# Performance work log

Measured on AMD Instinct MI355X. Metric: run time of the kernel, lower is better.

The kernel has to match this reference:

```python
import jax, jax.numpy as jnp
import numpy as np
from jax import lax

BATCH = 8192
HID = 10
IN = 64
STEPS = 512
REVERSE = True


def setup_inputs() -> dict:
    key = jax.random.key(0)
    ks = jax.random.split(key, 9)
    s_in = 1.0 / np.sqrt(HID)
    return {
        "hidden": jax.random.normal(ks[0], (1, BATCH, HID), dtype=jnp.float32),
        "w_ih": jax.random.uniform(ks[1], (3 * HID, IN), jnp.float32, -s_in, s_in),
        "w_hh": jax.random.uniform(ks[2], (3 * HID, HID), jnp.float32, -s_in, s_in),
        "b_ih": jax.random.uniform(ks[3], (3 * HID,), jnp.float32, -s_in, s_in),
        "b_hh": jax.random.uniform(ks[4], (3 * HID,), jnp.float32, -s_in, s_in),
        "l1_w": jax.random.uniform(ks[5], (10, HID), jnp.float32, -s_in, s_in),
        "l1_b": jax.random.uniform(ks[6], (10,), jnp.float32, -s_in, s_in),
        "l2_w": jax.random.uniform(ks[7], (IN, 10), jnp.float32, -s_in, s_in),
        "l2_b": jax.random.uniform(ks[8], (IN,), jnp.float32, -s_in, s_in),
        "step": STEPS,
    }


def _gru_cell(h, x, w_ih, w_hh, b_ih, b_hh):
    # PyTorch GRU gate order: reset, update, new
    gi = x @ w_ih.T + b_ih  # [B, 3H]
    gh = h @ w_hh.T + b_hh  # [B, 3H]
    i_r, i_z, i_n = jnp.split(gi, 3, axis=-1)
    h_r, h_z, h_n = jnp.split(gh, 3, axis=-1)
    r = jax.nn.sigmoid(i_r + h_r)
    z = jax.nn.sigmoid(i_z + h_z)
    n = jnp.tanh(i_n + r * h_n)
    return (1.0 - z) * n + z * h


def reference(hidden, w_ih, w_hh, b_ih, b_hh, l1_w, l1_b, l2_w, l2_b, step):
    h0 = hidden[0]  # [B, H]
    B = h0.shape[0]
    x0 = jnp.zeros((B, IN), dtype=h0.dtype)  # first GRU input is zeros

    def body(carry, _):
        h, x = carry
        h_new = _gru_cell(h, x, w_ih, w_hh, b_ih, b_hh)
        o = h_new @ l1_w.T + l1_b          # l1 on GRU output
        x_next = o @ l2_w.T + l2_b         # l2 feeds next GRU step
        return (h_new, x_next), o

    _, outs = lax.scan(body, (h0, x0), None, length=step)  # [T, B, 10]
    outs = jnp.transpose(outs, (1, 0, 2))  # [B, T, 10]
    if REVERSE:
        outs = outs[:, ::-1, :]
    return outs
```

## Files before the change

### kernel.cpp

```cpp
#include <hip/hip_runtime.h>

#define HID 10
#define STEPS 512

typedef __attribute__((ext_vector_type(2))) float v2f;

template<int F>
static __device__ __forceinline__ float swz(float v) {
    return __int_as_float(__builtin_amdgcn_ds_swizzle(__float_as_int(v), (F << 5) | 0x10));
}

__global__ __launch_bounds__(64, 2) void gru_decoder_kernel(
    const float* __restrict__ hidden, const float* __restrict__ w_ih,
    const float* __restrict__ w_hh, const float* __restrict__ b_ih,
    const float* __restrict__ b_hh, const float* __restrict__ l1_w,
    const float* __restrict__ l1_b, const float* __restrict__ l2_w,
    const float* __restrict__ l2_b, float* __restrict__ out)
{
    __shared__ float sWx[640];
    __shared__ float sbx[64];
    __shared__ float sWgi[300];
    __shared__ float sbgi[30];
    __shared__ float sWhh[300];

    const int lane = threadIdx.x;
    const int f    = lane & 15;
    const int b    = blockIdx.x * 4 + (lane >> 4);
    const bool ok  = (f < HID);
    const int fi   = ok ? f : 0;

    for (int e = lane; e < 640; e += 64) {
        int i = e / 10, j = e - i * 10;
        float acc = 0.f;
        #pragma unroll
        for (int k = 0; k < 10; ++k) acc += l2_w[i * 10 + k] * l1_w[k * 10 + j];
        sWx[e] = acc;
    }
    {
        float acc = l2_b[lane];
        #pragma unroll
        for (int k = 0; k < 10; ++k) acc += l2_w[lane * 10 + k] * l1_b[k];
        sbx[lane] = acc;
    }
    for (int e = lane; e < 300; e += 64) sWhh[e] = w_hh[e];
    __syncthreads();
    for (int e = lane; e < 300; e += 64) {
        int m = e / 10, j = e - m * 10;
        float acc = 0.f;
        for (int k = 0; k < 64; ++k) acc += w_ih[m * 64 + k] * sWx[k * 10 + j];
        sWgi[e] = acc;
    }
    if (lane < 30) {
        float acc = b_ih[lane];
        for (int k = 0; k < 64; ++k) acc += w_ih[lane * 64 + k] * sbx[k];
        sbgi[lane] = acc;
    }
    __syncthreads();

    const float LOG2E = 1.4426950408889634f;
    const float S2    = 2.f * LOG2E;

    v2f wrz[10], wnn[10];
    float wo[10];
    #pragma unroll
    for (int k = 0; k < 10; ++k) {
        float grz_r = -(sWgi[fi * 10 + k] + sWhh[fi * 10 + k]) * LOG2E;
        float grz_z = -(sWgi[(10 + fi) * 10 + k] + sWhh[(10 + fi) * 10 + k]) * LOG2E;
        float gni   = sWgi[(20 + fi) * 10 + k] * S2;
        float gnh   = sWhh[(20 + fi) * 10 + k] * S2;
        wrz[k] = ok ? v2f{grz_r, grz_z} : v2f{0.f, 0.f};
        wnn[k] = ok ? v2f{gni, gnh} : v2f{0.f, 0.f};
        wo[k]  = ok ? l1_w[fi * 10 + k] : 0.f;
    }
    const v2f brz = ok ? v2f{-(sbgi[fi] + b_hh[fi]) * LOG2E,
                             -(sbgi[10 + fi] + b_hh[10 + fi]) * LOG2E}
                       : v2f{0.f, 0.f};
    const v2f bnn = ok ? v2f{sbgi[20 + fi] * S2, b_hh[20 + fi] * S2} : v2f{0.f, 0.f};
    const float bo = ok ? l1_b[fi] : 0.f;
    const v2f brz0 = ok ? v2f{-(b_ih[fi] + b_hh[fi]) * LOG2E,
                              -(b_ih[10 + fi] + b_hh[10 + fi]) * LOG2E}
                        : v2f{0.f, 0.f};
    const float bni0 = ok ? b_ih[20 + fi] * S2 : 0.f;

    float h = ok ? hidden[(size_t)b * HID + f] : 0.f;

    float ha[10];
    #define GATHER()                                                       \
        ha[0] = swz<0>(h); ha[1] = swz<1>(h); ha[2] = swz<2>(h);           \
        ha[3] = swz<3>(h); ha[4] = swz<4>(h); ha[5] = swz<5>(h);           \
        ha[6] = swz<6>(h); ha[7] = swz<7>(h); ha[8] = swz<8>(h);           \
        ha[9] = swz<9>(h);

    GATHER();

    float* pb = out + (size_t)b * (STEPS * HID) + (size_t)(STEPS - 1) * HID + f;

    #define O_AND_STORE()                                                  \
        {                                                                  \
            float o = bo;                                                  \
            _Pragma("unroll")                                              \
            for (int k = 0; k < 10; ++k) o += wo[k] * ha[k];               \
            if (ok) pb[0] = o;                                             \
            pb -= HID;                                                     \
        }

    {
        float pr = 0.f, pz = 0.f, ph = 0.f;
        #pragma unroll
        for (int k = 0; k < 10; ++k) {
            pr += sWhh[fi * 10 + k] * ha[k];
            pz += sWhh[(10 + fi) * 10 + k] * ha[k];
            ph += sWhh[(20 + fi) * 10 + k] * ha[k];
        }
        float vr = brz0.x - pr * LOG2E;
        float vz = brz0.y - pz * LOG2E;
        float r = __builtin_amdgcn_rcpf(1.f + __builtin_amdgcn_exp2f(vr));
        float z = __builtin_amdgcn_rcpf(1.f + __builtin_amdgcn_exp2f(vz));
        float y = bni0 + r * (ph * S2 + bnn.y);
        float n = 1.f - 2.f * __builtin_amdgcn_rcpf(1.f + __builtin_amdgcn_exp2f(y));
        h = ok ? (n + z * (h - n)) : 0.f;
        GATHER();
        O_AND_STORE();
    }

    #pragma unroll 1
    for (int t = 1; t < STEPS; ++t) {
        v2f arz = brz, ann = bnn;
        #pragma unroll
        for (int k = 0; k < 10; ++k) {
            v2f hh = {ha[k], ha[k]};
            arz += wrz[k] * hh;
            ann += wnn[k] * hh;
        }
        float r = __builtin_amdgcn_rcpf(1.f + __builtin_amdgcn_exp2f(arz.x));
        float z = __builtin_amdgcn_rcpf(1.f + __builtin_amdgcn_exp2f(arz.y));
        float y = ann.x + r * ann.y;
        float n = 1.f - 2.f * __builtin_amdgcn_rcpf(1.f + __builtin_amdgcn_exp2f(y));
        h = n + z * (h - n);
        GATHER();
        O_AND_STORE();
    }
}

extern "C" void kernel_launch(void* const* d_in, const int* in_sizes, int n_in,
                              void* d_out, int out_size, void* d_ws, size_t ws_size,
                              hipStream_t stream) {
    (void)in_sizes; (void)n_in; (void)d_ws; (void)ws_size; (void)out_size;
    dim3 grid(2048), block(64);
    gru_decoder_kernel<<<grid, block, 0, stream>>>(
        (const float*)d_in[0], (const float*)d_in[1], (const float*)d_in[2],
        (const float*)d_in[3], (const float*)d_in[4], (const float*)d_in[5],
        (const float*)d_in[6], (const float*)d_in[7], (const float*)d_in[8],
        (float*)d_out);
}
```

Baseline: 317.1 us.

## Pack two batch rows per 16-lane group with DPP rotations and merged GRU tail

Remaps lanes so each 16-lane group serves two batch rows: each lane owns one or two hidden features, so 8 lanes per row hold features 0-7 and two lanes also hold features 8-9. The hidden-state gather now uses DPP row rotations plus two ds_swizzles instead of ten ds_swizzles, and the weights are pre-permuted to match the rotation order. The output projection is folded into the same packed FMA chains, split into even and odd accumulators for more ILP, and the GRU tail merges the sigmoid and tanh reciprocals into a single reciprocal. The grid is halved and waves_per_eu is set to 1, trading occupancy for more registers and more work per lane, and the rewritten tail algebra may change numerical behaviour.

```diff
diff --git a/kernel.cpp b/kernel.cpp
--- a/kernel.cpp
+++ b/kernel.cpp
@@ -5,12 +5,23 @@
 
 typedef __attribute__((ext_vector_type(2))) float v2f;
 
-template<int F>
-static __device__ __forceinline__ float swz(float v) {
-    return __int_as_float(__builtin_amdgcn_ds_swizzle(__float_as_int(v), (F << 5) | 0x10));
-}
-
-__global__ __launch_bounds__(64, 2) void gru_decoder_kernel(
+template<int PAT>
+static __device__ __forceinline__ float dsw(float v) {
+    return __int_as_float(__builtin_amdgcn_ds_swizzle(__float_as_int(v), PAT));
+}
+
+template<int J>
+static __device__ __forceinline__ float frot(float v) {
+    return __int_as_float(__builtin_amdgcn_update_dpp(
+        0, __float_as_int(v), 0x120 + J, 0xF, 0xF, true));
+}
+template<int J>
+static __device__ __forceinline__ int irot(int v) {
+    return __builtin_amdgcn_update_dpp(0, v, 0x120 + J, 0xF, 0xF, true);
+}
+
+__attribute__((amdgpu_waves_per_eu(1, 1)))
+__global__ __launch_bounds__(64) void gru_decoder_kernel(
     const float* __restrict__ hidden, const float* __restrict__ w_ih,
     const float* __restrict__ w_hh, const float* __restrict__ b_ih,
     const float* __restrict__ b_hh, const float* __restrict__ l1_w,
@@ -24,10 +35,14 @@
     __shared__ float sWhh[300];
 
     const int lane = threadIdx.x;
-    const int f    = lane & 15;
-    const int b    = blockIdx.x * 4 + (lane >> 4);
-    const bool ok  = (f < HID);
-    const int fi   = ok ? f : 0;
+    const int sub  = lane & 15;
+    const int row  = lane >> 4;
+    const int p    = sub & 1;
+    const int s    = sub >> 1;
+    const int b    = blockIdx.x * 8 + row * 2 + p;
+    const int f0   = s;
+    const bool ok1 = (s < 2);
+    const int fi1  = ok1 ? (8 + s) : 8;
 
     for (int e = lane; e < 640; e += 64) {
         int i = e / 10, j = e - i * 10;
@@ -60,93 +75,164 @@
     const float LOG2E = 1.4426950408889634f;
     const float S2    = 2.f * LOG2E;
 
-    v2f wrz[10], wnn[10];
-    float wo[10];
+    int idx[8];
+    idx[0] = sub;
+    idx[1] = irot<2>(sub);  idx[2] = irot<4>(sub);  idx[3] = irot<6>(sub);
+    idx[4] = irot<8>(sub);  idx[5] = irot<10>(sub); idx[6] = irot<12>(sub);
+    idx[7] = irot<14>(sub);
+
+    auto WR = [&](int ff, int k) { return -(sWgi[ff * 10 + k] + sWhh[ff * 10 + k]) * LOG2E; };
+    auto WZ = [&](int ff, int k) { return -(sWgi[(10 + ff) * 10 + k] + sWhh[(10 + ff) * 10 + k]) * LOG2E; };
+    auto WI = [&](int ff, int k) { return sWgi[(20 + ff) * 10 + k] * S2; };
+    auto WH = [&](int ff, int k) { return sWhh[(20 + ff) * 10 + k] * S2; };
+
+    v2f wrz0[10], wih0[10], wrz1[10], wih1[10], woo[10];
     #pragma unroll
-    for (int k = 0; k < 10; ++k) {
-        float grz_r = -(sWgi[fi * 10 + k] + sWhh[fi * 10 + k]) * LOG2E;
-        float grz_z = -(sWgi[(10 + fi) * 10 + k] + sWhh[(10 + fi) * 10 + k]) * LOG2E;
-        float gni   = sWgi[(20 + fi) * 10 + k] * S2;
-        float gnh   = sWhh[(20 + fi) * 10 + k] * S2;
-        wrz[k] = ok ? v2f{grz_r, grz_z} : v2f{0.f, 0.f};
-        wnn[k] = ok ? v2f{gni, gnh} : v2f{0.f, 0.f};
-        wo[k]  = ok ? l1_w[fi * 10 + k] : 0.f;
-    }
-    const v2f brz = ok ? v2f{-(sbgi[fi] + b_hh[fi]) * LOG2E,
-                             -(sbgi[10 + fi] + b_hh[10 + fi]) * LOG2E}
-                       : v2f{0.f, 0.f};
-    const v2f bnn = ok ? v2f{sbgi[20 + fi] * S2, b_hh[20 + fi] * S2} : v2f{0.f, 0.f};
-    const float bo = ok ? l1_b[fi] : 0.f;
-    const v2f brz0 = ok ? v2f{-(b_ih[fi] + b_hh[fi]) * LOG2E,
-                              -(b_ih[10 + fi] + b_hh[10 + fi]) * LOG2E}
-                        : v2f{0.f, 0.f};
-    const float bni0 = ok ? b_ih[20 + fi] * S2 : 0.f;
-
-    float h = ok ? hidden[(size_t)b * HID + f] : 0.f;
-
-    float ha[10];
-    #define GATHER()                                                       \
-        ha[0] = swz<0>(h); ha[1] = swz<1>(h); ha[2] = swz<2>(h);           \
-        ha[3] = swz<3>(h); ha[4] = swz<4>(h); ha[5] = swz<5>(h);           \
-        ha[6] = swz<6>(h); ha[7] = swz<7>(h); ha[8] = swz<8>(h);           \
-        ha[9] = swz<9>(h);
-
-    GATHER();
-
-    float* pb = out + (size_t)b * (STEPS * HID) + (size_t)(STEPS - 1) * HID + f;
-
-    #define O_AND_STORE()                                                  \
-        {                                                                  \
-            float o = bo;                                                  \
-            _Pragma("unroll")                                              \
-            for (int k = 0; k < 10; ++k) o += wo[k] * ha[k];               \
-            if (ok) pb[0] = o;                                             \
-            pb -= HID;                                                     \
+    for (int j = 0; j < 10; ++j) {
+        int k = (j < 8) ? (idx[j] >> 1) : j;
+        wrz0[j] = v2f{WR(f0, k), WZ(f0, k)};
+        wih0[j] = v2f{WI(f0, k), WH(f0, k)};
+        wrz1[j] = ok1 ? v2f{WR(fi1, k), WZ(fi1, k)} : v2f{0.f, 0.f};
+        wih1[j] = ok1 ? v2f{WI(fi1, k), WH(fi1, k)} : v2f{0.f, 0.f};
+        woo[j]  = v2f{l1_w[f0 * 10 + k], ok1 ? l1_w[fi1 * 10 + k] : 0.f};
+    }
+    const v2f Brz0 = {-(sbgi[f0] + b_hh[f0]) * LOG2E,
+                      -(sbgi[10 + f0] + b_hh[10 + f0]) * LOG2E};
+    const v2f Bih0 = {sbgi[20 + f0] * S2, b_hh[20 + f0] * S2};
+    const v2f Brz1 = ok1 ? v2f{-(sbgi[fi1] + b_hh[fi1]) * LOG2E,
+                               -(sbgi[10 + fi1] + b_hh[10 + fi1]) * LOG2E}
+                         : v2f{0.f, 0.f};
+    const v2f Bih1 = ok1 ? v2f{sbgi[20 + fi1] * S2, b_hh[20 + fi1] * S2} : v2f{0.f, 0.f};
+    const v2f Boo  = {l1_b[f0], ok1 ? l1_b[fi1] : 0.f};
+    const float br0_0 = -(b_ih[f0] + b_hh[f0]) * LOG2E;
+    const float bz0_0 = -(b_ih[10 + f0] + b_hh[10 + f0]) * LOG2E;
+    const float bn0_0 = b_ih[20 + f0] * S2;
+    const float br0_1 = -(b_ih[fi1] + b_hh[fi1]) * LOG2E;
+    const float bz0_1 = -(b_ih[10 + fi1] + b_hh[10 + fi1]) * LOG2E;
+    const float bn0_1 = b_ih[20 + fi1] * S2;
+
+    float hx = hidden[(size_t)b * HID + f0];
+    float hy = ok1 ? hidden[(size_t)b * HID + fi1] : 0.f;
+
+    float* pb0 = out + (size_t)b * (STEPS * HID) + (size_t)(STEPS - 1) * HID + f0;
+    float* pb1 = out + (size_t)b * (STEPS * HID) + (size_t)(STEPS - 1) * HID + fi1;
+
+    auto tail = [&](float arx, float azx, float aix, float ahx, float h) {
+        float er = __builtin_amdgcn_exp2f(arx);
+        float r  = __builtin_amdgcn_rcpf(1.f + er);
+        float ez = __builtin_amdgcn_exp2f(azx);
+        float y  = __builtin_fmaf(r, ahx, aix);
+        float en = __builtin_amdgcn_exp2f(y);
+        float pp = en * ez;
+        float u  = pp + (h - ez);
+        float num = __builtin_fmaf(h, en, u);
+        float den = (pp + (en + ez)) + 1.f;
+        return num * __builtin_amdgcn_rcpf(den);
+    };
+
+    {
+        float g0 = hx,          g1 = frot<2>(hx),  g2 = frot<4>(hx),
+              g3 = frot<6>(hx), g4 = frot<8>(hx),  g5 = frot<10>(hx),
+              g6 = frot<12>(hx), g7 = frot<14>(hx);
+        float h8g = dsw<0x0011>(hy), h9g = dsw<0x0051>(hy);
+        float gv[8] = {g0, g1, g2, g3, g4, g5, g6, g7};
+        float pr0 = 0.f, pz0 = 0.f, ph0 = 0.f, pr1 = 0.f, pz1 = 0.f, ph1 = 0.f;
+        #pragma unroll
+        for (int j = 0; j < 8; ++j) {
+            int k = idx[j] >> 1;
+            float hv = gv[j];
+            pr0 += sWhh[f0 * 10 + k] * hv;
+            pz0 += sWhh[(10 + f0) * 10 + k] * hv;
+            ph0 += sWhh[(20 + f0) * 10 + k] * hv;
+            pr1 += sWhh[fi1 * 10 + k] * hv;
+            pz1 += sWhh[(10 + fi1) * 10 + k] * hv;
+            ph1 += sWhh[(20 + fi1) * 10 + k] * hv;
         }
-
-    {
-        float pr = 0.f, pz = 0.f, ph = 0.f;
-        #pragma unroll
-        for (int k = 0; k < 10; ++k) {
-            pr += sWhh[fi * 10 + k] * ha[k];
-            pz += sWhh[(10 + fi) * 10 + k] * ha[k];
-            ph += sWhh[(20 + fi) * 10 + k] * ha[k];
-        }
-        float vr = brz0.x - pr * LOG2E;
-        float vz = brz0.y - pz * LOG2E;
-        float r = __builtin_amdgcn_rcpf(1.f + __builtin_amdgcn_exp2f(vr));
-        float z = __builtin_amdgcn_rcpf(1.f + __builtin_amdgcn_exp2f(vz));
-        float y = bni0 + r * (ph * S2 + bnn.y);
-        float n = 1.f - 2.f * __builtin_amdgcn_rcpf(1.f + __builtin_amdgcn_exp2f(y));
-        h = ok ? (n + z * (h - n)) : 0.f;
-        GATHER();
-        O_AND_STORE();
-    }
+        pr0 += sWhh[f0 * 10 + 8] * h8g + sWhh[f0 * 10 + 9] * h9g;
+        pz0 += sWhh[(10 + f0) * 10 + 8] * h8g + sWhh[(10 + f0) * 10 + 9] * h9g;
+        ph0 += sWhh[(20 + f0) * 10 + 8] * h8g + sWhh[(20 + f0) * 10 + 9] * h9g;
+        pr1 += sWhh[fi1 * 10 + 8] * h8g + sWhh[fi1 * 10 + 9] * h9g;
+        pz1 += sWhh[(10 + fi1) * 10 + 8] * h8g + sWhh[(10 + fi1) * 10 + 9] * h9g;
+        ph1 += sWhh[(20 + fi1) * 10 + 8] * h8g + sWhh[(20 + fi1) * 10 + 9] * h9g;
+        hx = tail(br0_0 - pr0 * LOG2E, bz0_0 - pz0 * LOG2E,
+                  bn0_0, ph0 * S2 + b_hh[20 + f0] * S2, hx);
+        float ny = tail(br0_1 - pr1 * LOG2E, bz0_1 - pz1 * LOG2E,
+                        bn0_1, ph1 * S2 + b_hh[20 + fi1] * S2, hy);
+        hy = ok1 ? ny : 0.f;
+    }
+
+    #define HH(x) (v2f{(x), (x)})
 
     #pragma unroll 1
     for (int t = 1; t < STEPS; ++t) {
-        v2f arz = brz, ann = bnn;
-        #pragma unroll
-        for (int k = 0; k < 10; ++k) {
-            v2f hh = {ha[k], ha[k]};
-            arz += wrz[k] * hh;
-            ann += wnn[k] * hh;
-        }
-        float r = __builtin_amdgcn_rcpf(1.f + __builtin_amdgcn_exp2f(arz.x));
-        float z = __builtin_amdgcn_rcpf(1.f + __builtin_amdgcn_exp2f(arz.y));
-        float y = ann.x + r * ann.y;
-        float n = 1.f - 2.f * __builtin_amdgcn_rcpf(1.f + __builtin_amdgcn_exp2f(y));
-        h = n + z * (h - n);
-        GATHER();
-        O_AND_STORE();
-    }
+        float h8g = dsw<0x0011>(hy);
+        float h9g = dsw<0x0051>(hy);
+        float g0 = hx,          g1 = frot<2>(hx),  g2 = frot<4>(hx),
+              g3 = frot<6>(hx), g4 = frot<8>(hx),  g5 = frot<10>(hx),
+              g6 = frot<12>(hx), g7 = frot<14>(hx);
+
+        v2f aE0 = wrz0[0] * HH(g0) + Brz0;  v2f aO0 = wrz0[1] * HH(g1);
+        v2f bE0 = wih0[0] * HH(g0) + Bih0;  v2f bO0 = wih0[1] * HH(g1);
+        v2f aE1 = wrz1[0] * HH(g0) + Brz1;  v2f aO1 = wrz1[1] * HH(g1);
+        v2f bE1 = wih1[0] * HH(g0) + Bih1;  v2f bO1 = wih1[1] * HH(g1);
+        v2f oE  = woo[0]  * HH(g0) + Boo;   v2f oO  = woo[1]  * HH(g1);
+        aE0 += wrz0[2] * HH(g2);  aO0 += wrz0[3] * HH(g3);
+        bE0 += wih0[2] * HH(g2);  bO0 += wih0[3] * HH(g3);
+        aE1 += wrz1[2] * HH(g2);  aO1 += wrz1[3] * HH(g3);
+        bE1 += wih1[2] * HH(g2);  bO1 += wih1[3] * HH(g3);
+        oE  += woo[2]  * HH(g2);  oO  += woo[3]  * HH(g3);
+        aE0 += wrz0[4] * HH(g4);  aO0 += wrz0[5] * HH(g5);
+        bE0 += wih0[4] * HH(g4);  bO0 += wih0[5] * HH(g5);
+        aE1 += wrz1[4] * HH(g4);  aO1 += wrz1[5] * HH(g5);
+        bE1 += wih1[4] * HH(g4);  bO1 += wih1[5] * HH(g5);
+        oE  += woo[4]  * HH(g4);  oO  += woo[5]  * HH(g5);
+        aE0 += wrz0[6] * HH(g6);  aO0 += wrz0[7] * HH(g7);
+        bE0 += wih0[6] * HH(g6);  bO0 += wih0[7] * HH(g7);
+        aE1 += wrz1[6] * HH(g6);  aO1 += wrz1[7] * HH(g7);
+        bE1 += wih1[6] * HH(g6);  bO1 += wih1[7] * HH(g7);
+        oE  += woo[6]  * HH(g6);  oO  += woo[7]  * HH(g7);
+        aE0 += wrz0[8] * HH(h8g); aO0 += wrz0[9] * HH(h9g);
+        bE0 += wih0[8] * HH(h8g); bO0 += wih0[9] * HH(h9g);
+        aE1 += wrz1[8] * HH(h8g); aO1 += wrz1[9] * HH(h9g);
+        bE1 += wih1[8] * HH(h8g); bO1 += wih1[9] * HH(h9g);
+        oE  += woo[8]  * HH(h8g); oO  += woo[9]  * HH(h9g);
+
+        v2f arz0 = aE0 + aO0;
+        v2f aih0 = bE0 + bO0;
+        v2f arz1 = aE1 + aO1;
+        v2f aih1 = bE1 + bO1;
+        v2f ao   = oE + oO;
+
+        hx = tail(arz0.x, arz0.y, aih0.x, aih0.y, hx);
+        hy = tail(arz1.x, arz1.y, aih1.x, aih1.y, hy);
+
+        pb0[0] = ao.x;
+        if (ok1) pb1[0] = ao.y;
+        pb0 -= HID; pb1 -= HID;
+    }
+
+    {
+        float h8g = dsw<0x0011>(hy), h9g = dsw<0x0051>(hy);
+        float g0 = hx,          g1 = frot<2>(hx),  g2 = frot<4>(hx),
+              g3 = frot<6>(hx), g4 = frot<8>(hx),  g5 = frot<10>(hx),
+              g6 = frot<12>(hx), g7 = frot<14>(hx);
+        v2f oE = woo[0] * HH(g0) + Boo;  v2f oO = woo[1] * HH(g1);
+        oE += woo[2] * HH(g2);  oO += woo[3] * HH(g3);
+        oE += woo[4] * HH(g4);  oO += woo[5] * HH(g5);
+        oE += woo[6] * HH(g6);  oO += woo[7] * HH(g7);
+        oE += woo[8] * HH(h8g); oO += woo[9] * HH(h9g);
+        v2f ao = oE + oO;
+        pb0[0] = ao.x;
+        if (ok1) pb1[0] = ao.y;
+    }
+    #undef HH
 }
 
 extern "C" void kernel_launch(void* const* d_in, const int* in_sizes, int n_in,
                               void* d_out, int out_size, void* d_ws, size_t ws_size,
                               hipStream_t stream) {
     (void)in_sizes; (void)n_in; (void)d_ws; (void)ws_size; (void)out_size;
-    dim3 grid(2048), block(64);
+    dim3 grid(1024), block(64);
     gru_decoder_kernel<<<grid, block, 0, stream>>>(
         (const float*)d_in[0], (const float*)d_in[1], (const float*)d_in[2],
         (const float*)d_in[3], (const float*)d_in[4], (const float*)d_in[5],
```

Measured after the change: 346.0 us. +9.1%, slower.
